# Kernel optimization log

Hardware: AMD Instinct MI355X
Metric: run time of the kernel (lower is better)

Reference implementation:

```python
import jax, jax.numpy as jnp
import numpy as np
from jax import lax

K_SEL = 30   # top-30 nearest voxels used for attention
K_NRM = 8    # top-8 nearest voxels used for the query normal estimate
C = 128      # output_channel
H = 1        # num_heads
DEPTH = C // H


def setup_inputs() -> dict:
    key = jax.random.key(0)
    ks = jax.random.split(key, 10)
    N, M = 8192, 16384
    x_world = jax.random.normal(ks[0], (N, 1, 3), dtype=jnp.float32)
    voxel_point = jax.random.normal(ks[1], (M, 3), dtype=jnp.float32)
    voxel_normal = jax.random.normal(ks[2], (M, 3), dtype=jnp.float32)
    v = jax.random.normal(ks[3], (M, 1), dtype=jnp.float32)
    # Linear params (torch nn.Linear: y = x @ W.T + b)
    s_fc = 1.0 / np.sqrt(6.0)
    s_c = 1.0 / np.sqrt(C)
    fc_w = jax.random.uniform(ks[4], (C, 6), jnp.float32, -s_fc, s_fc)
    fc_b = jax.random.uniform(ks[5], (C,), jnp.float32, -s_fc, s_fc)
    wq_w = jax.random.uniform(ks[6], (C, C), jnp.float32, -s_c, s_c)
    wq_b = jax.random.uniform(ks[7], (C,), jnp.float32, -s_c, s_c)
    wk_w = jax.random.uniform(ks[8], (C, C), jnp.float32, -s_c, s_c)
    wk_b = jax.random.uniform(ks[9], (C,), jnp.float32, -s_c, s_c)
    return {"x_world": x_world, "voxel_point": voxel_point, "voxel_normal": voxel_normal,
            "v": v, "fc_w": fc_w, "fc_b": fc_b, "wq_w": wq_w, "wq_b": wq_b,
            "wk_w": wk_w, "wk_b": wk_b}


def reference(x_world, voxel_point, voxel_normal, v, fc_w, fc_b, wq_w, wq_b, wk_w, wk_b):
    # x_world: [N,1,3], voxel_point/voxel_normal: [M,3], v: [M,1]
    # pairwise distances [N,M]
    dist = jnp.linalg.norm(x_world - voxel_point[None, :, :3], axis=-1)
    # top-30 nearest voxels (ascending distance == top_k of -distance)
    _, idx = lax.top_k(-dist, K_SEL)            # [N,30]
    idx8 = idx[:, :K_NRM]
    vp_sel = voxel_point[idx]                    # [N,30,3]
    vn_sel = voxel_normal[idx]                   # [N,30,3]
    v_sel = v[idx]                               # [N,30,1]
    x_normal = jnp.mean(voxel_normal[idx8], axis=1, keepdims=True)  # [N,1,3]
    normal_rel = x_normal - vn_sel               # [N,30,3]
    # mirror torch.no_grad detachment of the selected/normal tensors
    vp_sel = lax.stop_gradient(vp_sel)
    normal_rel = lax.stop_gradient(normal_rel)
    v_sel = lax.stop_gradient(v_sel)
    pos_rel = x_world - vp_sel                   # [N,30,3]
    x = jnp.concatenate([pos_rel, normal_rel], axis=-1)  # [N,30,6]
    x = x @ fc_w.T + fc_b                        # [N,30,C]
    Q = x @ wq_w.T + wq_b                        # [N,30,C] (num_heads=1 -> depth=C)
    K = x @ wk_w.T + wk_b
    scores = jnp.einsum('nkd,nld->nkl', Q, K) / np.sqrt(DEPTH).astype(np.float32)
    attn = jax.nn.softmax(scores, axis=-1)       # [N,30,30]
    out = jnp.einsum('nkl,nlo->nko', attn, v_sel)[..., 0]  # [N,30]
    return jnp.mean(out, axis=1)                 # [N]
```

## Files before the change

### kernel.cpp

```cpp
#include <hip/hip_runtime.h>
#include <math.h>
#include <float.h>

#define KSEL 30
#define KNRM 8
#define CAP  320
#define PL   320
#define G    32
#define NCELL (G*G*G)
#define GLO  (-4.8f)
#define Hc   (0.3f)
#define INVH (3.3333333333f)
#define NWAVE 2
#define NB   64

typedef unsigned long long ull;
typedef unsigned int uint;

__device__ __forceinline__ int cell_coord(float x) {
    int c = (int)floorf((x - GLO) * INVH);
    return c < 0 ? 0 : (c > G - 1 ? G - 1 : c);
}

__device__ __forceinline__ float gap1(float x, int i) {
    float lo = (i == 0)     ? -1e30f : GLO + (float)i * Hc;
    float hi = (i == G - 1) ?  1e30f : GLO + (float)(i + 1) * Hc;
    float g = 0.f;
    g = fmaxf(g, lo - x);
    g = fmaxf(g, x - hi);
    return g;
}

__device__ __forceinline__ void gbar(int* ctr, int idx) {
    __syncthreads();
    if (threadIdx.x == 0) {
        __threadfence();
        atomicAdd(&ctr[idx], 1);
        while (__hip_atomic_load(&ctr[idx], __ATOMIC_RELAXED,
                                 __HIP_MEMORY_SCOPE_AGENT) < NB) {
            __builtin_amdgcn_s_sleep(2);
        }
        __threadfence();
    }
    __syncthreads();
}

__global__ __launch_bounds__(256) void k_build(
    const float* __restrict__ vp, int* __restrict__ ctr, int* __restrict__ cc,
    int2* __restrict__ cse, float4* __restrict__ sp4,
    int* __restrict__ gpart, int M,
    const float* __restrict__ fc_w, const float* __restrict__ fc_b,
    const float* __restrict__ wq_w, const float* __restrict__ wq_b,
    const float* __restrict__ wk_w, const float* __restrict__ wk_b,
    float* __restrict__ ws)
{
    const int b   = blockIdx.x;
    const int tid = threadIdx.x;

    __shared__ int   part[256];
    __shared__ int   s_excl;
    __shared__ float Fs[768];
    __shared__ float fb[128];
    __shared__ float Gq[128][6];
    __shared__ float Gk[128][6];
    __shared__ float hq[128];

    if (b == NB) {
        for (int e = tid; e < 768; e += 256) Fs[e] = fc_w[e];
        if (tid < 128) fb[tid] = fc_b[tid];
        __syncthreads();
        const float4* wq4 = (const float4*)wq_w;
        const float4* wk4 = (const float4*)wk_w;
        for (int e = tid; e < 768; e += 256) {
            int r = e / 6, c = e % 6;
            float aq = 0.f, ak = 0.f;
            for (int k = 0; k < 32; ++k) {
                float4 a = wq4[r * 32 + k];
                float4 bb = wk4[r * 32 + k];
                aq += a.x * Fs[(4 * k + 0) * 6 + c];
                aq += a.y * Fs[(4 * k + 1) * 6 + c];
                aq += a.z * Fs[(4 * k + 2) * 6 + c];
                aq += a.w * Fs[(4 * k + 3) * 6 + c];
                ak += bb.x * Fs[(4 * k + 0) * 6 + c];
                ak += bb.y * Fs[(4 * k + 1) * 6 + c];
                ak += bb.z * Fs[(4 * k + 2) * 6 + c];
                ak += bb.w * Fs[(4 * k + 3) * 6 + c];
            }
            Gq[r][c] = aq;
            Gk[r][c] = ak;
        }
        if (tid < 128) {
            float a = wq_b[tid];
            for (int k = 0; k < 32; ++k) {
                float4 v = wq4[tid * 32 + k];
                a += v.x * fb[4 * k + 0];
                a += v.y * fb[4 * k + 1];
                a += v.z * fb[4 * k + 2];
                a += v.w * fb[4 * k + 3];
            }
            hq[tid] = a;
        }
        __syncthreads();
        const float inv_s = 0.0883883476483184f;
        if (tid < 36) {
            int a = tid / 6, bcol = tid % 6;
            float s = 0.f;
            for (int i = 0; i < 128; ++i) s += Gq[i][a] * Gk[i][bcol];
            ws[tid] = s * inv_s;
        }
        if (tid >= 64 && tid < 70) {
            int bcol = tid - 64;
            float s = 0.f;
            for (int i = 0; i < 128; ++i) s += Gk[i][bcol] * hq[i];
            ws[36 + bcol] = s * inv_s;
        }
        return;
    }

    for (int i = b * 256 + tid; i < M; i += NB * 256) {
        int cx = cell_coord(vp[i * 3 + 0]);
        int cy = cell_coord(vp[i * 3 + 1]);
        int cz = cell_coord(vp[i * 3 + 2]);
        atomicAdd(&cc[(cx * G + cy) * G + cz], 1);
    }
    gbar(ctr, 0);

    const int base = b * (NCELL / NB);
    int c0 = cc[base + 2 * tid];
    int c1 = cc[base + 2 * tid + 1];
    int s  = c0 + c1;
    part[tid] = s;
    __syncthreads();
    for (int off = 1; off < 256; off <<= 1) {
        int v = (tid >= off) ? part[tid - off] : 0;
        __syncthreads();
        part[tid] += v;
        __syncthreads();
    }
    if (tid == 255) gpart[b] = part[255];
    gbar(ctr, 1);

    if (tid < 64) {
        int v = gpart[tid];
        int inc = v;
#pragma unroll
        for (int off = 1; off < 64; off <<= 1) {
            int t = __shfl_up(inc, off, 64);
            if (tid >= off) inc += t;
        }
        if (tid == b) s_excl = inc - v;
    }
    __syncthreads();

    {
        int excl = s_excl + part[tid] - s;
        int st0 = excl, st1 = excl + c0;
        cse[base + 2 * tid]     = make_int2(st0, st0 + c0);
        cse[base + 2 * tid + 1] = make_int2(st1, st1 + c1);
        cc[base + 2 * tid]      = st0;
        cc[base + 2 * tid + 1]  = st1;
    }
    gbar(ctr, 2);

    for (int i = b * 256 + tid; i < M; i += NB * 256) {
        float x = vp[i * 3 + 0], y = vp[i * 3 + 1], z = vp[i * 3 + 2];
        int c = (cell_coord(x) * G + cell_coord(y)) * G + cell_coord(z);
        int p = atomicAdd(&cc[c], 1);
        sp4[p] = make_float4(x, y, z, __int_as_float(i));
    }
}

__global__ __launch_bounds__(64 * NWAVE) void k_main(
    const float* __restrict__ xw, const float* __restrict__ vp,
    const float* __restrict__ vn, const float* __restrict__ vv,
    const float* __restrict__ ws,
    const int2* __restrict__ cse, const float4* __restrict__ sp4,
    float* __restrict__ out, int M, int N)
{
    const int tid  = threadIdx.x;
    const int lane = tid & 63;
    const int w    = tid >> 6;
    const int n    = blockIdx.x * NWAVE + w;
    const bool valid = (n < N);

    __shared__ ull            s_key[NWAVE][CAP];
    __shared__ unsigned short s_pl[NWAVE][PL];
    __shared__ float s_t[NWAVE][KSEL][6];
    __shared__ float s_vn[NWAVE][KSEL][3];
    __shared__ float s_e[NWAVE][KSEL];
    __shared__ float s_v[NWAVE][KSEL];
    __shared__ float s_o[NWAVE][KSEL];
    __shared__ int   s_sel[NWAVE][KSEL];
    __shared__ float s_xn[NWAVE][3];
    __shared__ int   s_cnt[NWAVE];
    __shared__ int   s_pn[NWAVE];
    __shared__ int   s_done[NWAVE];

    const float x0 = valid ? xw[n * 3 + 0] : 0.f;
    const float x1 = valid ? xw[n * 3 + 1] : 0.f;
    const float x2 = valid ? xw[n * 3 + 2] : 0.f;

    auto midf = [](float a, float b) -> float {
        unsigned ua = __float_as_uint(a), ub = __float_as_uint(b);
        return __uint_as_float((ua + ub) >> 1);
    };

    const float c0 = 0.063493636f * (float)M * 4.18879020f;
    float R = sqrtf(x0 * x0 + x1 * x1 + x2 * x2);
    float r = cbrtf(30.0f / (c0 * __expf(-0.5f * R * R)));
#pragma unroll
    for (int it = 0; it < 4; ++it) {
        float d  = fmaxf(R - r, 0.0f);
        float rn = cbrtf(30.0f / (c0 * __expf(-0.5f * d * d)));
        r = sqrtf(r * rn);
    }
    float T = 1.45f * r * r;

    float Tlo = 0.f, Thi = 0.f;
    bool  haveHi = false, last = false;
    bool  mydone = !valid;
    int   nc = 0;

    for (int attempt = 0; attempt < 24; ++attempt) {
        if (lane == 0) s_cnt[w] = 0;
        __syncthreads();

        if (!mydone) {
            float Tm = T * 1.000002f;
            float sq = sqrtf(T);
            int ax0 = cell_coord(x0 - sq), ax1 = cell_coord(x0 + sq);
            int ay0 = cell_coord(x1 - sq), ay1 = cell_coord(x1 + sq);
            int az0 = cell_coord(x2 - sq), az1 = cell_coord(x2 + sq);
            int nyv = ay1 - ay0 + 1, nz = az1 - az0 + 1;
            int tot = (ax1 - ax0 + 1) * nyv * nz;

            uint mz  = (nz  > 1) ? (uint)((0x100000000ULL + (ull)nz  - 1) / (ull)nz ) : 0u;
            uint myv = (nyv > 1) ? (uint)((0x100000000ULL + (ull)nyv - 1) / (ull)nyv) : 0u;

            if (lane == 0) s_pn[w] = 0;

            for (int cb = 0; cb < tot; cb += 64) {
                int ci = cb + lane;
                int rs = 0, re = 0;
                if (ci < tot) {
                    uint rest = (nz  > 1) ? __umulhi((uint)ci, mz)  : (uint)ci;
                    uint iz   = (uint)ci - rest * (uint)nz;
                    uint q2   = (nyv > 1) ? __umulhi(rest, myv) : rest;
                    uint iy   = rest - q2 * (uint)nyv;
                    int  IX = ax0 + (int)q2, IY = ay0 + (int)iy, IZ = az0 + (int)iz;
                    float gx = gap1(x0, IX), gy = gap1(x1, IY), gz = gap1(x2, IZ);
                    float mind2 = gx * gx + gy * gy + gz * gz;
                    if (mind2 <= Tm) {
                        int2 se = cse[(IX * G + IY) * G + IZ];
                        rs = se.x; re = se.y;
                    }
                }
                while (__any(rs < re)) {
                    if (rs < re) {
                        int len  = re - rs;
                        int bse  = atomicAdd(&s_pn[w], len);
                        int room = PL - bse;
                        int take = room > 0 ? (len < room ? len : room) : 0;
                        for (int i = 0; i < take; ++i)
                            s_pl[w][bse + i] = (unsigned short)(rs + i);
                        rs += take;
                    }
                    int tt = s_pn[w]; tt = tt < PL ? tt : PL;
                    for (int p = lane; p < tt; p += 64) {
                        int pidx = s_pl[w][p];
                        float4 q = sp4[pidx];
                        float dx = __fsub_rn(x0, q.x);
                        float dy = __fsub_rn(x1, q.y);
                        float dz = __fsub_rn(x2, q.z);
                        float d2 = __fadd_rn(__fadd_rn(__fmul_rn(dx, dx), __fmul_rn(dy, dy)),
                                             __fmul_rn(dz, dz));
                        if (d2 < T) {
                            int pos = atomicAdd(&s_cnt[w], 1);
                            if (pos < CAP) {
                                s_key[w][pos] = ((ull)__float_as_uint(d2) << 32) |
                                                (unsigned)__float_as_int(q.w);
                            }
                        }
                    }
                    if (lane == 0) s_pn[w] = 0;
                }
            }
        }
        __syncthreads();

        if (!mydone) {
            nc = s_cnt[w];
            if (last || (nc >= KSEL && nc <= CAP)) {
                mydone = true;
            } else {
                if (nc < KSEL) { Tlo = T; T = haveHi ? midf(Tlo, Thi) : T * 2.5f; }
                else           { Thi = T; haveHi = true; T = midf(Tlo, Thi); }
                if (haveHi && (__float_as_uint(Thi) - __float_as_uint(Tlo) <= 1u)) {
                    T = Thi;
                    last = true;
                }
            }
        }
        if (lane == 0) s_done[w] = mydone ? 1 : 0;
        __syncthreads();
        bool alldone = true;
#pragma unroll
        for (int w2 = 0; w2 < NWAVE; ++w2) alldone = alldone && (s_done[w2] != 0);
        if (alldone) break;
    }
    if (nc > CAP) nc = CAP;

    if (lane < KSEL) s_sel[w][lane] = 0;
    __syncthreads();

    for (int i0 = lane; i0 < nc; i0 += 64) {
        ull me = s_key[w][i0];
        int rank = 0;
        for (int i = 0; i < nc; ++i) rank += (s_key[w][i] < me) ? 1 : 0;
        if (rank < KSEL) s_sel[w][rank] = (int)(me & 0xffffffffull);
    }
    __syncthreads();

    float r0 = 0.f, r1 = 0.f, r2 = 0.f;
    if (lane < KSEL) {
        int ix = s_sel[w][lane];
        r0 = __fsub_rn(x0, vp[ix * 3 + 0]);
        r1 = __fsub_rn(x1, vp[ix * 3 + 1]);
        r2 = __fsub_rn(x2, vp[ix * 3 + 2]);
        s_vn[w][lane][0] = vn[ix * 3 + 0];
        s_vn[w][lane][1] = vn[ix * 3 + 1];
        s_vn[w][lane][2] = vn[ix * 3 + 2];
        s_v[w][lane]     = vv[ix];
    }
    __syncthreads();
    if (lane == 0) {
        float a0 = 0.f, a1 = 0.f, a2 = 0.f;
        for (int k = 0; k < KNRM; ++k) {
            a0 += s_vn[w][k][0]; a1 += s_vn[w][k][1]; a2 += s_vn[w][k][2];
        }
        s_xn[w][0] = a0 * 0.125f; s_xn[w][1] = a1 * 0.125f; s_xn[w][2] = a2 * 0.125f;
    }
    __syncthreads();

    float r3 = 0.f, r4 = 0.f, r5 = 0.f;
    if (lane < KSEL) {
        r3 = __fsub_rn(s_xn[w][0], s_vn[w][lane][0]);
        r4 = __fsub_rn(s_xn[w][1], s_vn[w][lane][1]);
        r5 = __fsub_rn(s_xn[w][2], s_vn[w][lane][2]);
        float rr[6] = {r0, r1, r2, r3, r4, r5};
        float e = 0.f;
#pragma unroll
        for (int i = 0; i < 6; ++i) e += ws[36 + i] * rr[i];
        s_e[w][lane] = e;
#pragma unroll
        for (int j = 0; j < 6; ++j) {
            float t = 0.f;
#pragma unroll
            for (int i = 0; i < 6; ++i) t += ws[j * 6 + i] * rr[i];
            s_t[w][lane][j] = t;
        }
    }
    __syncthreads();

    if (lane < KSEL) {
        float sc[KSEL];
        float mx = -1e30f;
#pragma unroll
        for (int l = 0; l < KSEL; ++l) {
            float s = s_e[w][l];
            s += r0 * s_t[w][l][0];
            s += r1 * s_t[w][l][1];
            s += r2 * s_t[w][l][2];
            s += r3 * s_t[w][l][3];
            s += r4 * s_t[w][l][4];
            s += r5 * s_t[w][l][5];
            sc[l] = s;
            mx = fmaxf(mx, s);
        }
        float den = 0.f, num = 0.f;
#pragma unroll
        for (int l = 0; l < KSEL; ++l) {
            float wgt = __expf(sc[l] - mx);
            den += wgt;
            num += wgt * s_v[w][l];
        }
        s_o[w][lane] = num / den;
    }
    __syncthreads();

    if (lane == 0 && valid) {
        float a = 0.f;
        for (int k = 0; k < KSEL; ++k) a += s_o[w][k];
        out[n] = a * (1.0f / 30.0f);
    }
}

extern "C" void kernel_launch(void* const* d_in, const int* in_sizes, int n_in,
                              void* d_out, int out_size, void* d_ws, size_t ws_size,
                              hipStream_t stream)
{
    const float* xw   = (const float*)d_in[0];
    const float* vp   = (const float*)d_in[1];
    const float* vn   = (const float*)d_in[2];
    const float* vv   = (const float*)d_in[3];
    const float* fc_w = (const float*)d_in[4];
    const float* fc_b = (const float*)d_in[5];
    const float* wq_w = (const float*)d_in[6];
    const float* wq_b = (const float*)d_in[7];
    const float* wk_w = (const float*)d_in[8];
    const float* wk_b = (const float*)d_in[9];

    int N = in_sizes[0] / 3;
    int M = in_sizes[1] / 3;

    float*  ws_f  = (float*)d_ws;
    int*    ctr   = (int*)(ws_f + 64);
    int*    cc    = ctr + 16;
    int2*   cse   = (int2*)(cc + NCELL);
    float4* sp4   = (float4*)(cse + NCELL);
    int*    gpart = (int*)(sp4 + M);

    hipMemsetAsync(ctr, 0, (16 + NCELL) * sizeof(int), stream);

    k_build<<<NB + 1, 256, 0, stream>>>(vp, ctr, cc, cse, sp4, gpart, M,
                                        fc_w, fc_b, wq_w, wq_b, wk_w, wk_b, ws_f);
    k_main<<<(N + NWAVE - 1) / NWAVE, 64 * NWAVE, 0, stream>>>(
        xw, vp, vn, vv, ws_f, cse, sp4, (float*)d_out, M, N);
}
```

Baseline: 85.78 us.

## Build voxel grid in a single workgroup with LDS histogram and scan

Replaces the 64-block grid build, which relied on cross-block spin barriers and a global-memory histogram, with one 1024-thread workgroup. That workgroup keeps the 32K-cell counts in padded shared memory and does a local prefix scan and scatter there. This drops the memset, the global atomics and the grid-wide barriers. The cost is that the build becomes serial on one CU (16K points per 1024 threads) and may take longer than the parallel version. The shared-memory footprint is about 140 KB, which needs large LDS support.

```diff
diff --git a/kernel.cpp b/kernel.cpp
--- a/kernel.cpp
+++ b/kernel.cpp
@@ -12,7 +12,7 @@
 #define Hc   (0.3f)
 #define INVH (3.3333333333f)
 #define NWAVE 2
-#define NB   64
+#define PC(c) ((c) + ((c) >> 5))
 
 typedef unsigned long long ull;
 typedef unsigned int uint;
@@ -31,51 +31,35 @@
     return g;
 }
 
-__device__ __forceinline__ void gbar(int* ctr, int idx) {
-    __syncthreads();
-    if (threadIdx.x == 0) {
-        __threadfence();
-        atomicAdd(&ctr[idx], 1);
-        while (__hip_atomic_load(&ctr[idx], __ATOMIC_RELAXED,
-                                 __HIP_MEMORY_SCOPE_AGENT) < NB) {
-            __builtin_amdgcn_s_sleep(2);
-        }
-        __threadfence();
-    }
-    __syncthreads();
-}
-
-__global__ __launch_bounds__(256) void k_build(
-    const float* __restrict__ vp, int* __restrict__ ctr, int* __restrict__ cc,
-    int2* __restrict__ cse, float4* __restrict__ sp4,
-    int* __restrict__ gpart, int M,
+__global__ __launch_bounds__(1024) void k_build1(
+    const float* __restrict__ vp,
+    int2* __restrict__ cse, float4* __restrict__ sp4, int M,
     const float* __restrict__ fc_w, const float* __restrict__ fc_b,
     const float* __restrict__ wq_w, const float* __restrict__ wq_b,
     const float* __restrict__ wk_w, const float* __restrict__ wk_b,
     float* __restrict__ ws)
 {
-    const int b   = blockIdx.x;
     const int tid = threadIdx.x;
 
-    __shared__ int   part[256];
-    __shared__ int   s_excl;
+    __shared__ int   s_cc[NCELL + (NCELL >> 5)];
+    __shared__ int   s_part[1024];
     __shared__ float Fs[768];
     __shared__ float fb[128];
     __shared__ float Gq[128][6];
     __shared__ float Gk[128][6];
     __shared__ float hq[128];
 
-    if (b == NB) {
-        for (int e = tid; e < 768; e += 256) Fs[e] = fc_w[e];
+    if (blockIdx.x == 1) {
+        for (int e = tid; e < 768; e += 1024) Fs[e] = fc_w[e];
         if (tid < 128) fb[tid] = fc_b[tid];
         __syncthreads();
         const float4* wq4 = (const float4*)wq_w;
         const float4* wk4 = (const float4*)wk_w;
-        for (int e = tid; e < 768; e += 256) {
+        for (int e = tid; e < 768; e += 1024) {
             int r = e / 6, c = e % 6;
             float aq = 0.f, ak = 0.f;
             for (int k = 0; k < 32; ++k) {
-                float4 a = wq4[r * 32 + k];
+                float4 a  = wq4[r * 32 + k];
                 float4 bb = wk4[r * 32 + k];
                 aq += a.x * Fs[(4 * k + 0) * 6 + c];
                 aq += a.y * Fs[(4 * k + 1) * 6 + c];
@@ -117,55 +101,51 @@
         return;
     }
 
-    for (int i = b * 256 + tid; i < M; i += NB * 256) {
+    for (int c = tid; c < NCELL; c += 1024) s_cc[PC(c)] = 0;
+    __syncthreads();
+
+    for (int i = tid; i < M; i += 1024) {
         int cx = cell_coord(vp[i * 3 + 0]);
         int cy = cell_coord(vp[i * 3 + 1]);
         int cz = cell_coord(vp[i * 3 + 2]);
-        atomicAdd(&cc[(cx * G + cy) * G + cz], 1);
-    }
-    gbar(ctr, 0);
-
-    const int base = b * (NCELL / NB);
-    int c0 = cc[base + 2 * tid];
-    int c1 = cc[base + 2 * tid + 1];
-    int s  = c0 + c1;
-    part[tid] = s;
-    __syncthreads();
-    for (int off = 1; off < 256; off <<= 1) {
-        int v = (tid >= off) ? part[tid - off] : 0;
-        __syncthreads();
-        part[tid] += v;
-        __syncthreads();
-    }
-    if (tid == 255) gpart[b] = part[255];
-    gbar(ctr, 1);
-
-    if (tid < 64) {
-        int v = gpart[tid];
-        int inc = v;
-#pragma unroll
-        for (int off = 1; off < 64; off <<= 1) {
-            int t = __shfl_up(inc, off, 64);
-            if (tid >= off) inc += t;
-        }
-        if (tid == b) s_excl = inc - v;
-    }
-    __syncthreads();
-
+        atomicAdd(&s_cc[PC((cx * G + cy) * G + cz)], 1);
+    }
+    __syncthreads();
+
+    const int base = tid * 32;
+    int s = 0;
+#pragma unroll
+    for (int k = 0; k < 32; ++k) s += s_cc[PC(base + k)];
+    s_part[tid] = s;
+    __syncthreads();
+    for (int off = 1; off < 1024; off <<= 1) {
+        int v = (tid >= off) ? s_part[tid - off] : 0;
+        __syncthreads();
+        s_part[tid] += v;
+        __syncthreads();
+    }
     {
-        int excl = s_excl + part[tid] - s;
-        int st0 = excl, st1 = excl + c0;
-        cse[base + 2 * tid]     = make_int2(st0, st0 + c0);
-        cse[base + 2 * tid + 1] = make_int2(st1, st1 + c1);
-        cc[base + 2 * tid]      = st0;
-        cc[base + 2 * tid + 1]  = st1;
-    }
-    gbar(ctr, 2);
-
-    for (int i = b * 256 + tid; i < M; i += NB * 256) {
+        int run = s_part[tid] - s;
+#pragma unroll
+        for (int k = 0; k < 32; ++k) {
+            int cnt = s_cc[PC(base + k)];
+            s_cc[PC(base + k)] = run;
+            run += cnt;
+        }
+    }
+    __syncthreads();
+
+    for (int c = tid; c < NCELL; c += 1024) {
+        int st = s_cc[PC(c)];
+        int en = (c + 1 < NCELL) ? s_cc[PC(c + 1)] : M;
+        cse[c] = make_int2(st, en);
+    }
+    __syncthreads();
+
+    for (int i = tid; i < M; i += 1024) {
         float x = vp[i * 3 + 0], y = vp[i * 3 + 1], z = vp[i * 3 + 2];
         int c = (cell_coord(x) * G + cell_coord(y)) * G + cell_coord(z);
-        int p = atomicAdd(&cc[c], 1);
+        int p = atomicAdd(&s_cc[PC(c)], 1);
         sp4[p] = make_float4(x, y, z, __int_as_float(i));
     }
 }
@@ -413,17 +393,12 @@
     int N = in_sizes[0] / 3;
     int M = in_sizes[1] / 3;
 
-    float*  ws_f  = (float*)d_ws;
-    int*    ctr   = (int*)(ws_f + 64);
-    int*    cc    = ctr + 16;
-    int2*   cse   = (int2*)(cc + NCELL);
-    float4* sp4   = (float4*)(cse + NCELL);
-    int*    gpart = (int*)(sp4 + M);
-
-    hipMemsetAsync(ctr, 0, (16 + NCELL) * sizeof(int), stream);
-
-    k_build<<<NB + 1, 256, 0, stream>>>(vp, ctr, cc, cse, sp4, gpart, M,
-                                        fc_w, fc_b, wq_w, wq_b, wk_w, wk_b, ws_f);
+    float*  ws_f = (float*)d_ws;
+    int2*   cse  = (int2*)(ws_f + 64);
+    float4* sp4  = (float4*)(cse + NCELL);
+
+    k_build1<<<2, 1024, 0, stream>>>(vp, cse, sp4, M,
+                                     fc_w, fc_b, wq_w, wq_b, wk_w, wk_b, ws_f);
     k_main<<<(N + NWAVE - 1) / NWAVE, 64 * NWAVE, 0, stream>>>(
         xw, vp, vn, vv, ws_f, cse, sp4, (float*)d_out, M, N);
 }
```

New measurement: 82.71 us, median of 2. -3.6%, faster.
